# Kernel optimization log

Measured on AMD Instinct MI355X. Metric: run time of the kernel, lower is better.

Reference implementation:

```python
import jax, jax.numpy as jnp
import numpy as np

GROUPS = 4
KLD_SCALE = 10.0
COMMIT_COST = 0.25


def setup_inputs() -> dict:
    key = jax.random.key(0)
    k1, k2, k3, k4 = jax.random.split(key, 4)
    B, H, C = 8, 4096, 512
    n_embed, d = 512, C // GROUPS
    return {
        "z": jax.random.normal(k1, (B, H, C), dtype=jnp.float32),
        "embed_w": jax.random.normal(k2, (n_embed, d), dtype=jnp.float32),
        "proj_w": jax.random.normal(k3, (C, C), dtype=jnp.float32) * (1.0 / np.sqrt(C)),
        "proj_b": jax.random.normal(k4, (C,), dtype=jnp.float32) * 0.01,
    }


def reference(z, embed_w, proj_w, proj_b):
    B, H, C = z.shape
    d = C // GROUPS
    sg = jax.lax.stop_gradient
    # split channels into groups -> [B, H*groups, d]
    z_e = z.reshape(B, H * GROUPS, d)
    flat = z_e.reshape(-1, d)  # [N, d]
    dist = ((flat ** 2).sum(1, keepdims=True)
            - 2.0 * flat @ embed_w.T
            + (embed_w ** 2).sum(1)[None, :])  # [N, n_embed]
    ind = jnp.argmin(dist, axis=1).reshape(B, H * GROUPS)  # (-dist).max == dist.min
    z_q = embed_w[ind]  # [B, H*groups, d]
    diff = KLD_SCALE * (COMMIT_COST * jnp.mean((sg(z_q) - z_e) ** 2)
                        + jnp.mean((z_q - sg(z_e)) ** 2))
    # straight-through estimator
    z_q = z_e + sg(z_q - z_e)
    z_q = z_q.reshape(B, H, C)
    out = z_q @ proj_w.T + proj_b
    return out, diff, ind
```

## Files before the change

kernel.cpp:

```cpp
#include <hip/hip_runtime.h>

constexpr int D         = 128;
constexpr int NE        = 512;
constexpr int NROWS     = 131072;
constexpr int CC        = 512;
constexpr int OUT_ELEMS = 16777216;


using half8  = __attribute__((ext_vector_type(8))) _Float16;
using f32x16 = __attribute__((ext_vector_type(16))) float;

#define F16_MINNORM 6.103515625e-05f

__global__ void eprep_kernel(const float* __restrict__ embed,
                             unsigned short* __restrict__ esw,
                             float* __restrict__ entab,
                             float* __restrict__ ws_diff) {
    const int chunk = blockIdx.x;
    const int tid = threadIdx.x;
    const int cl = tid >> 3;
    const int seg = tid & 7;
    const float* src = embed + (size_t)(chunk * 32 + cl) * D + seg * 16;
    unsigned short* cb = esw + (size_t)chunk * 8192;

    float ss = 0.f;
#pragma unroll
    for (int g2 = 0; g2 < 2; g2++) {
        float4 a = ((const float4*)src)[g2 * 2 + 0];
        float4 b = ((const float4*)src)[g2 * 2 + 1];
        float v[8] = {a.x, a.y, a.z, a.w, b.x, b.y, b.z, b.w};
        half8 t1, t2;
#pragma unroll
        for (int i = 0; i < 8; i++) {
            ss += v[i] * v[i];
            float m2 = -2.0f * v[i];
            float m2c = (__builtin_fabsf(m2) < F16_MINNORM) ? 0.0f : m2;
            _Float16 h = (_Float16)m2c;
            float r = m2 - (float)h;
            t1[i] = h;
            t2[i] = (_Float16)(r * 2048.0f);
        }
        const int idx = seg * 512 + g2 * 256 + cl * 8;
        *(half8*)(cb + idx) = t1;
        *(half8*)(cb + 4096 + idx) = t2;
    }
    ss += __shfl_down(ss, 4, 8);
    ss += __shfl_down(ss, 2, 8);
    ss += __shfl_down(ss, 1, 8);
    if (seg == 0) entab[chunk * 32 + cl] = ss;
    if (chunk == 0 && tid == 0) ws_diff[0] = 0.0f;
}

#define AS_STRIDE 68
#define AS_S4 17

__launch_bounds__(256, 4)
__global__ void pgemm_kernel(const float* __restrict__ embed,
                             const float* __restrict__ projw,
                             float* __restrict__ P) {
    __shared__ float As[64 * AS_STRIDE];
    __shared__ float Bs[64 * AS_STRIDE];
    const int tid = threadIdx.x;
    const int cbase = blockIdx.x * 64;
    const int jbase = blockIdx.y * 64;
    const int g = blockIdx.z;
    const int tx = tid & 15, ty = tid >> 4;
    const int r = tid >> 2, seg = tid & 3;

    float acc[4][4];
#pragma unroll
    for (int i = 0; i < 4; i++)
#pragma unroll
        for (int j = 0; j < 4; j++) acc[i][j] = 0.f;

    for (int kb = 0; kb < D; kb += 64) {
        const float4* asrc = (const float4*)(embed + (size_t)(jbase + r) * D + kb + seg * 16);
        const float4* bsrc = (const float4*)(projw + (size_t)(cbase + r) * CC + g * D + kb + seg * 16);
        float4* adst = (float4*)&As[r * AS_STRIDE + seg * 16];
        float4* bdst = (float4*)&Bs[r * AS_STRIDE + seg * 16];
#pragma unroll
        for (int q = 0; q < 4; q++) { adst[q] = asrc[q]; bdst[q] = bsrc[q]; }
        __syncthreads();

        const float4* as4 = (const float4*)As;
        const float4* bs4 = (const float4*)Bs;
#pragma unroll 4
        for (int kk = 0; kk < 16; kk++) {
            float4 a[4], b[4];
#pragma unroll
            for (int i = 0; i < 4; i++) a[i] = as4[(ty + 16 * i) * AS_S4 + kk];
#pragma unroll
            for (int j = 0; j < 4; j++) b[j] = bs4[(tx + 16 * j) * AS_S4 + kk];
#pragma unroll
            for (int i = 0; i < 4; i++)
#pragma unroll
                for (int j = 0; j < 4; j++)
                    acc[i][j] += a[i].x * b[j].x + a[i].y * b[j].y +
                                 a[i].z * b[j].z + a[i].w * b[j].w;
        }
        __syncthreads();
    }
#pragma unroll
    for (int j = 0; j < 4; j++) {
#pragma unroll
        for (int i = 0; i < 4; i++)
            P[(size_t)g * 262144 + (size_t)(jbase + ty + 16 * i) * CC + cbase + tx + 16 * j] =
                acc[i][j];
    }
}

__global__ __launch_bounds__(256, 2)
void argmin_mfma_kernel(const float* __restrict__ z,
                        const unsigned short* __restrict__ esw,
                        const float* __restrict__ entab,
                        float* __restrict__ ws_diff,
                        float* __restrict__ ind_f) {
    __shared__ unsigned char ebuf[32768];
    const int tid = threadIdx.x;
    const int lane = tid & 63;
    const int wave = tid >> 6;
    const int h5 = lane >> 5, l5 = lane & 31;
    const int rb = blockIdx.x * 256 + wave * 64;

    half8 x1[2][8], x2[2][8];
    float xn[2];
#pragma unroll
    for (int s = 0; s < 2; s++) {
        const float* zr = z + (size_t)(rb + s * 32 + l5) * D + h5 * 8;
        float ss = 0.f;
#pragma unroll
        for (int kk = 0; kk < 8; kk++) {
            float4 a = *(const float4*)(zr + kk * 16);
            float4 b = *(const float4*)(zr + kk * 16 + 4);
            float v[8] = {a.x, a.y, a.z, a.w, b.x, b.y, b.z, b.w};
            half8 t1, t2;
#pragma unroll
            for (int i = 0; i < 8; i++) {
                ss += v[i] * v[i];
                float vc = (__builtin_fabsf(v[i]) < F16_MINNORM) ? 0.0f : v[i];
                _Float16 h = (_Float16)vc;
                float r = v[i] - (float)h;
                t1[i] = h;
                t2[i] = (_Float16)(r * 2048.0f);
            }
            x1[s][kk] = t1; x2[s][kk] = t2;
        }
        xn[s] = ss;
    }

    float minv[2] = {3.0e38f, 3.0e38f};
    int   mini[2] = {0, 0};

    auto stage = [&](int c, int b) {
        const unsigned char* s = (const unsigned char*)esw + (size_t)c * 16384 +
                                 wave * 4096 + lane * 16;
        unsigned char* d = &ebuf[b * 16384 + wave * 4096];
#pragma unroll
        for (int it = 0; it < 4; it++)
            __builtin_amdgcn_global_load_lds(
                (const __attribute__((address_space(1))) unsigned int*)(s + it * 1024),
                (__attribute__((address_space(3))) unsigned int*)(d + it * 1024),
                16, 0, 0);
    };

    stage(0, 0);
    __syncthreads();

#pragma unroll 1
    for (int c = 0; c < 16; c++) {
        if (c < 15) stage(c + 1, (c + 1) & 1);
        const unsigned char* ldsb = &ebuf[(c & 1) * 16384];

        float4 enr[4];
#pragma unroll
        for (int u = 0; u < 4; u++)
            enr[u] = *(const float4*)(entab + c * 32 + h5 * 4 + u * 8);

        f32x16 accA0 = (f32x16)(0.0f), accA1 = (f32x16)(0.0f);
        f32x16 accB0 = (f32x16)(0.0f), accB1 = (f32x16)(0.0f);
#pragma unroll
        for (int kk = 0; kk < 8; kk++) {
            const int fo = kk * 1024 + h5 * 512 + l5 * 16;
            half8 e1 = *(const half8*)(ldsb + fo);
            half8 e2 = *(const half8*)(ldsb + 8192 + fo);
            accA0 = __builtin_amdgcn_mfma_f32_32x32x16_f16(e1, x1[0][kk], accA0, 0, 0, 0);
            accA1 = __builtin_amdgcn_mfma_f32_32x32x16_f16(e1, x1[1][kk], accA1, 0, 0, 0);
            accB0 = __builtin_amdgcn_mfma_f32_32x32x16_f16(e1, x2[0][kk], accB0, 0, 0, 0);
            accB1 = __builtin_amdgcn_mfma_f32_32x32x16_f16(e1, x2[1][kk], accB1, 0, 0, 0);
            accB0 = __builtin_amdgcn_mfma_f32_32x32x16_f16(e2, x1[0][kk], accB0, 0, 0, 0);
            accB1 = __builtin_amdgcn_mfma_f32_32x32x16_f16(e2, x1[1][kk], accB1, 0, 0, 0);
        }

        const int cb2 = c * 32 + h5 * 4;
#pragma unroll
        for (int r = 0; r < 16; r++) {
            const float en = ((const float*)&enr[r >> 2])[r & 3];
            const int cand = cb2 + (r & 3) + 8 * (r >> 2);
            float d0 = fmaf(accB0[r], 4.8828125e-4f, accA0[r]) + en;
            float d1 = fmaf(accB1[r], 4.8828125e-4f, accA1[r]) + en;
            if (d0 < minv[0]) { minv[0] = d0; mini[0] = cand; }
            if (d1 < minv[1]) { minv[1] = d1; mini[1] = cand; }
        }
        __syncthreads();
    }

#pragma unroll
    for (int s = 0; s < 2; s++) {
        float ov = __shfl_xor(minv[s], 32);
        int oi = __shfl_xor(mini[s], 32);
        if (ov < minv[s] || (ov == minv[s] && oi < mini[s])) { minv[s] = ov; mini[s] = oi; }
    }
    if (lane < 32) {
        ind_f[rb + l5] = (float)mini[0];
        ind_f[rb + 32 + l5] = (float)mini[1];
    }

    float xf0 = xn[0] + __shfl_xor(xn[0], 32);
    float xf1 = xn[1] + __shfl_xor(xn[1], 32);
    float v = (lane < 32) ? (xf0 + minv[0] + xf1 + minv[1]) : 0.0f;
#pragma unroll
    for (int off = 32; off; off >>= 1) v += __shfl_down(v, off);
    if (lane == 0) atomicAdd(ws_diff, v);
}

__global__ void apply_kernel(const float* __restrict__ P,
                             const float* __restrict__ projb,
                             const float* __restrict__ ind_f,
                             float* __restrict__ out) {
    const int tid = threadIdx.x;
    const int m = blockIdx.x * 2 + (tid >> 7);
    const int c4 = tid & 127;

    const float4* pb4 = (const float4*)projb;
    float4 acc = pb4[c4];
    const float4* P4 = (const float4*)P;
#pragma unroll
    for (int g = 0; g < 4; g++) {
        const int ig = (int)ind_f[m * 4 + g];
        float4 p = P4[(size_t)g * 65536 + (size_t)ig * 128 + c4];
        acc.x += p.x; acc.y += p.y; acc.z += p.z; acc.w += p.w;
    }
    ((float4*)out)[(size_t)m * 128 + c4] = acc;
}

__global__ void finalize_kernel(const float* __restrict__ ws_diff,
                                float* __restrict__ diff_out) {
    diff_out[0] = 12.5f * ws_diff[0] * (1.0f / 16777216.0f);
}

extern "C" void kernel_launch(void* const* d_in, const int* in_sizes, int n_in,
                              void* d_out, int out_size, void* d_ws, size_t ws_size,
                              hipStream_t stream) {
    const float* z     = (const float*)d_in[0];
    const float* embed = (const float*)d_in[1];
    const float* projw = (const float*)d_in[2];
    const float* projb = (const float*)d_in[3];

    float* out      = (float*)d_out;
    float* diff_out = out + OUT_ELEMS;
    float* ind_f    = out + OUT_ELEMS + 1;

    char* wsb = (char*)d_ws;
    float* ws_diff = (float*)wsb;
    float* entab = (float*)(wsb + 1024);
    unsigned short* esw = (unsigned short*)(wsb + 4096);
    float* P = (float*)(wsb + 266240);

    eprep_kernel<<<16, 256, 0, stream>>>(embed, esw, entab, ws_diff);
    pgemm_kernel<<<dim3(8, 8, 4), 256, 0, stream>>>(embed, projw, P);
    argmin_mfma_kernel<<<NROWS / 256, 256, 0, stream>>>(z, esw, entab, ws_diff, ind_f);
    apply_kernel<<<32768 / 2, 256, 0, stream>>>(P, projb, ind_f, out);
    finalize_kernel<<<1, 1, 0, stream>>>(ws_diff, diff_out);
}
```

Measured before the change: 230.2 us.

## Fuse gather-projection into argmin kernel and halve rows per wave

Merges the separate apply kernel into the argmin kernel. Code indices now stay in shared memory and each block writes its 32 output rows directly, with no separate launch and no reread of indices from global memory. Each wave now handles 32 rows instead of 64, which halves register use and allows 3 blocks per CU instead of 2, doubling the block count. The cost is that each block restages the full codebook for only half as many rows, so codebook LDS traffic per row doubles.

```diff
diff --git a/kernel.cpp b/kernel.cpp
--- a/kernel.cpp
+++ b/kernel.cpp
@@ -109,25 +109,27 @@
     }
 }
 
-__global__ __launch_bounds__(256, 2)
-void argmin_mfma_kernel(const float* __restrict__ z,
-                        const unsigned short* __restrict__ esw,
-                        const float* __restrict__ entab,
-                        float* __restrict__ ws_diff,
-                        float* __restrict__ ind_f) {
+__global__ __launch_bounds__(256, 3)
+void argmin_fused_kernel(const float* __restrict__ z,
+                         const unsigned short* __restrict__ esw,
+                         const float* __restrict__ entab,
+                         const float* __restrict__ P,
+                         const float* __restrict__ projb,
+                         float* __restrict__ ws_diff,
+                         float* __restrict__ ind_f,
+                         float* __restrict__ out) {
     __shared__ unsigned char ebuf[32768];
+    __shared__ int ind_s[128];
     const int tid = threadIdx.x;
     const int lane = tid & 63;
     const int wave = tid >> 6;
     const int h5 = lane >> 5, l5 = lane & 31;
-    const int rb = blockIdx.x * 256 + wave * 64;
-
-    half8 x1[2][8], x2[2][8];
-    float xn[2];
-#pragma unroll
-    for (int s = 0; s < 2; s++) {
-        const float* zr = z + (size_t)(rb + s * 32 + l5) * D + h5 * 8;
-        float ss = 0.f;
+    const int rb = blockIdx.x * 128 + wave * 32;
+
+    half8 x1[8], x2[8];
+    float xn = 0.f;
+    {
+        const float* zr = z + (size_t)(rb + l5) * D + h5 * 8;
 #pragma unroll
         for (int kk = 0; kk < 8; kk++) {
             float4 a = *(const float4*)(zr + kk * 16);
@@ -136,20 +138,19 @@
             half8 t1, t2;
 #pragma unroll
             for (int i = 0; i < 8; i++) {
-                ss += v[i] * v[i];
+                xn += v[i] * v[i];
                 float vc = (__builtin_fabsf(v[i]) < F16_MINNORM) ? 0.0f : v[i];
                 _Float16 h = (_Float16)vc;
                 float r = v[i] - (float)h;
                 t1[i] = h;
                 t2[i] = (_Float16)(r * 2048.0f);
             }
-            x1[s][kk] = t1; x2[s][kk] = t2;
-        }
-        xn[s] = ss;
-    }
-
-    float minv[2] = {3.0e38f, 3.0e38f};
-    int   mini[2] = {0, 0};
+            x1[kk] = t1; x2[kk] = t2;
+        }
+    }
+
+    float minv = 3.0e38f;
+    int   mini = 0;
 
     auto stage = [&](int c, int b) {
         const unsigned char* s = (const unsigned char*)esw + (size_t)c * 16384 +
@@ -176,19 +177,15 @@
         for (int u = 0; u < 4; u++)
             enr[u] = *(const float4*)(entab + c * 32 + h5 * 4 + u * 8);
 
-        f32x16 accA0 = (f32x16)(0.0f), accA1 = (f32x16)(0.0f);
-        f32x16 accB0 = (f32x16)(0.0f), accB1 = (f32x16)(0.0f);
+        f32x16 accA = (f32x16)(0.0f), accB = (f32x16)(0.0f);
 #pragma unroll
         for (int kk = 0; kk < 8; kk++) {
             const int fo = kk * 1024 + h5 * 512 + l5 * 16;
             half8 e1 = *(const half8*)(ldsb + fo);
             half8 e2 = *(const half8*)(ldsb + 8192 + fo);
-            accA0 = __builtin_amdgcn_mfma_f32_32x32x16_f16(e1, x1[0][kk], accA0, 0, 0, 0);
-            accA1 = __builtin_amdgcn_mfma_f32_32x32x16_f16(e1, x1[1][kk], accA1, 0, 0, 0);
-            accB0 = __builtin_amdgcn_mfma_f32_32x32x16_f16(e1, x2[0][kk], accB0, 0, 0, 0);
-            accB1 = __builtin_amdgcn_mfma_f32_32x32x16_f16(e1, x2[1][kk], accB1, 0, 0, 0);
-            accB0 = __builtin_amdgcn_mfma_f32_32x32x16_f16(e2, x1[0][kk], accB0, 0, 0, 0);
-            accB1 = __builtin_amdgcn_mfma_f32_32x32x16_f16(e2, x1[1][kk], accB1, 0, 0, 0);
+            accA = __builtin_amdgcn_mfma_f32_32x32x16_f16(e1, x1[kk], accA, 0, 0, 0);
+            accB = __builtin_amdgcn_mfma_f32_32x32x16_f16(e1, x2[kk], accB, 0, 0, 0);
+            accB = __builtin_amdgcn_mfma_f32_32x32x16_f16(e2, x1[kk], accB, 0, 0, 0);
         }
 
         const int cb2 = c * 32 + h5 * 4;
@@ -196,51 +193,47 @@
         for (int r = 0; r < 16; r++) {
             const float en = ((const float*)&enr[r >> 2])[r & 3];
             const int cand = cb2 + (r & 3) + 8 * (r >> 2);
-            float d0 = fmaf(accB0[r], 4.8828125e-4f, accA0[r]) + en;
-            float d1 = fmaf(accB1[r], 4.8828125e-4f, accA1[r]) + en;
-            if (d0 < minv[0]) { minv[0] = d0; mini[0] = cand; }
-            if (d1 < minv[1]) { minv[1] = d1; mini[1] = cand; }
+            float d0 = fmaf(accB[r], 4.8828125e-4f, accA[r]) + en;
+            if (d0 < minv) { minv = d0; mini = cand; }
         }
         __syncthreads();
     }
 
-#pragma unroll
-    for (int s = 0; s < 2; s++) {
-        float ov = __shfl_xor(minv[s], 32);
-        int oi = __shfl_xor(mini[s], 32);
-        if (ov < minv[s] || (ov == minv[s] && oi < mini[s])) { minv[s] = ov; mini[s] = oi; }
+    {
+        float ov = __shfl_xor(minv, 32);
+        int oi = __shfl_xor(mini, 32);
+        if (ov < minv || (ov == minv && oi < mini)) { minv = ov; mini = oi; }
     }
     if (lane < 32) {
-        ind_f[rb + l5] = (float)mini[0];
-        ind_f[rb + 32 + l5] = (float)mini[1];
-    }
-
-    float xf0 = xn[0] + __shfl_xor(xn[0], 32);
-    float xf1 = xn[1] + __shfl_xor(xn[1], 32);
-    float v = (lane < 32) ? (xf0 + minv[0] + xf1 + minv[1]) : 0.0f;
+        ind_f[rb + l5] = (float)mini;
+        ind_s[wave * 32 + l5] = mini;
+    }
+
+    float xfull = xn + __shfl_xor(xn, 32);
+    float v = (lane < 32) ? (xfull + minv) : 0.0f;
 #pragma unroll
     for (int off = 32; off; off >>= 1) v += __shfl_down(v, off);
     if (lane == 0) atomicAdd(ws_diff, v);
-}
-
-__global__ void apply_kernel(const float* __restrict__ P,
-                             const float* __restrict__ projb,
-                             const float* __restrict__ ind_f,
-                             float* __restrict__ out) {
-    const int tid = threadIdx.x;
-    const int m = blockIdx.x * 2 + (tid >> 7);
+
+    __syncthreads();
+
+    const int mb = blockIdx.x * 32;
     const int c4 = tid & 127;
-
-    const float4* pb4 = (const float4*)projb;
-    float4 acc = pb4[c4];
+    const int mh = (tid >> 7) * 16;
+    const float4 bias = ((const float4*)projb)[c4];
     const float4* P4 = (const float4*)P;
-#pragma unroll
-    for (int g = 0; g < 4; g++) {
-        const int ig = (int)ind_f[m * 4 + g];
-        float4 p = P4[(size_t)g * 65536 + (size_t)ig * 128 + c4];
-        acc.x += p.x; acc.y += p.y; acc.z += p.z; acc.w += p.w;
-    }
-    ((float4*)out)[(size_t)m * 128 + c4] = acc;
+#pragma unroll 4
+    for (int u = 0; u < 16; u++) {
+        const int ml = mh + u;
+        float4 acc = bias;
+#pragma unroll
+        for (int g = 0; g < 4; g++) {
+            const int ig = ind_s[ml * 4 + g];
+            float4 p = P4[(size_t)g * 65536 + (size_t)ig * 128 + c4];
+            acc.x += p.x; acc.y += p.y; acc.z += p.z; acc.w += p.w;
+        }
+        ((float4*)out)[(size_t)(mb + ml) * 128 + c4] = acc;
+    }
 }
 
 __global__ void finalize_kernel(const float* __restrict__ ws_diff,
@@ -268,7 +261,7 @@
 
     eprep_kernel<<<16, 256, 0, stream>>>(embed, esw, entab, ws_diff);
     pgemm_kernel<<<dim3(8, 8, 4), 256, 0, stream>>>(embed, projw, P);
-    argmin_mfma_kernel<<<NROWS / 256, 256, 0, stream>>>(z, esw, entab, ws_diff, ind_f);
-    apply_kernel<<<32768 / 2, 256, 0, stream>>>(P, projb, ind_f, out);
+    argmin_fused_kernel<<<NROWS / 128, 256, 0, stream>>>(z, esw, entab, P, projb,
+                                                         ws_diff, ind_f, out);
     finalize_kernel<<<1, 1, 0, stream>>>(ws_diff, diff_out);
 }
```

After: 218.9 us. -4.9%, faster.
